# Kernel tuning notes

Hardware: AMD Instinct MI355X
Metric: run time of the kernel (lower is better)

Reference implementation:

```python
import jax, jax.numpy as jnp
import numpy as np

EPS = 1e-4

def mp_normalize(x, axis):
    # normalize() from the source: divisor = eps + ||x|| * sqrt(n_norm_elems / n_elems)
    # alpha = sqrt(norm.numel()/x.numel()) = 1/sqrt(prod of reduced dims)
    red = int(np.prod([x.shape[a] for a in axis])) if isinstance(axis, (list, tuple)) else x.shape[axis]
    w = jnp.sqrt(jnp.sum(jnp.square(x.astype(jnp.float32)), axis=axis, keepdims=True))
    w = EPS + w / np.sqrt(red)
    return x / w.astype(x.dtype)

def mp_linear(x, w, gain):
    # MP_Conv with (1,1) kernel == per-token linear; w: [out, in]
    fan_in = w.shape[1]
    wn = mp_normalize(w.astype(jnp.float32), axis=(1,)) * (gain / np.sqrt(fan_in))
    return jnp.einsum('bse,oe->bso', x, wn.astype(x.dtype))

def attention(query, gain, w_q, w_k, w_v, w_o, num_heads=16, attn_balance=0.5):
    B, S, E = query.shape
    hd = E // num_heads
    res = query
    q = mp_linear(query, w_q, gain).reshape(B, S, num_heads, hd).transpose(0, 2, 1, 3)  # bnsh
    k = mp_linear(query, w_k, gain).reshape(B, S, num_heads, hd).transpose(0, 2, 1, 3)
    v = mp_linear(query, w_v, gain).reshape(B, S, num_heads, hd).transpose(0, 2, 1, 3)
    q = mp_normalize(q, axis=(3,))
    k = mp_normalize(k, axis=(3,))
    # NOTE: contracts over sequence axis -> [B, H, hd, hd] (faithful to source einsum)
    scores = jnp.einsum('bnsh,bnsk->bnhk', q, k / np.sqrt(S))
    attn = jax.nn.softmax(scores, axis=3)
    o = jnp.einsum('bnhk,bnsk->bnsh', attn, v)  # [B, H, S, hd]
    o = o.transpose(0, 2, 1, 3).reshape(B, S, E)
    out = mp_linear(o, w_o, gain)
    t = attn_balance
    return (res * (1.0 - t) + out * t) / np.sqrt((1 - t) ** 2 + t ** 2)

def setup_inputs() -> dict:
    key = jax.random.key(0)
    ks = jax.random.split(key, 5)
    B, S, E = 4, 4096, 1024
    return {
        'query': jax.random.normal(ks[0], (B, S, E), dtype=jnp.float32),
        'gain': jnp.float32(1.0),
        'w_q': jax.random.normal(ks[1], (E, E), dtype=jnp.float32),
        'w_k': jax.random.normal(ks[2], (E, E), dtype=jnp.float32),
        'w_v': jax.random.normal(ks[3], (E, E), dtype=jnp.float32),
        'w_o': jax.random.normal(ks[4], (E, E), dtype=jnp.float32),
    }

def reference(query, gain, w_q, w_k, w_v, w_o):
    return attention(query, gain, w_q, w_k, w_v, w_o)
```

## Files before the change

### kernel.cpp

```cpp
#include <hip/hip_runtime.h>
#include <math.h>


typedef __bf16 bf16;
typedef __bf16 bf16x8 __attribute__((ext_vector_type(8)));
typedef __bf16 bf16x4 __attribute__((ext_vector_type(4)));
typedef float  f32x4  __attribute__((ext_vector_type(4)));

#define DEVINL __device__ __forceinline__

DEVINL void gload_lds16(const void* g, void* l) {
  __builtin_amdgcn_global_load_lds(
      (__attribute__((address_space(1))) void*)(void*)g,
      (__attribute__((address_space(3))) void*)l, 16, 0, 0);
}

static constexpr int Sq = 4096;
static constexpr int Ek = 1024;
static constexpr int Mrows = 16384;

__global__ __launch_bounds__(256) void k_prep_w(
    const float* __restrict__ wq, const float* __restrict__ wk,
    const float* __restrict__ wv, const float* __restrict__ wo,
    const float* __restrict__ gain_p,
    bf16* __restrict__ WN, bf16* __restrict__ WNO) {
  int r = blockIdx.x;
  int mat = r >> 10, row = r & 1023;
  const float* w = (mat == 0) ? wq : (mat == 1) ? wk : (mat == 2) ? wv : wo;
  int t = threadIdx.x;
  f32x4 v = *(const f32x4*)&w[(size_t)row * 1024 + t * 4];
  float ss = v[0]*v[0] + v[1]*v[1] + v[2]*v[2] + v[3]*v[3];
#pragma unroll
  for (int m2 = 1; m2 < 64; m2 <<= 1) ss += __shfl_xor(ss, m2);
  __shared__ float red[4];
  if ((t & 63) == 0) red[t >> 6] = ss;
  __syncthreads();
  float tot = red[0] + red[1] + red[2] + red[3];
  float g = gain_p[0];
  float scale = (g * 0.03125f) / (1e-4f + sqrtf(tot) * 0.03125f);
  bf16x4 ov;
  ov[0] = (bf16)(v[0]*scale); ov[1] = (bf16)(v[1]*scale);
  ov[2] = (bf16)(v[2]*scale); ov[3] = (bf16)(v[3]*scale);
  if (mat < 3) *(bf16x4*)&WN [(size_t)r   * 1024 + t * 4] = ov;
  else         *(bf16x4*)&WNO[(size_t)row * 1024 + t * 4] = ov;
}

__global__ __launch_bounds__(256) void k_cvt_x(const float* __restrict__ x,
                                               bf16* __restrict__ xb) {
  size_t idx = (size_t)blockIdx.x * 256 + threadIdx.x;
  const size_t n8 = (size_t)Mrows * Ek / 8;
  for (size_t i = idx; i < n8; i += (size_t)2048 * 256) {
    f32x4 a = *(const f32x4*)&x[i * 8];
    f32x4 b = *(const f32x4*)&x[i * 8 + 4];
    bf16x8 ov;
    ov[0]=(bf16)a[0]; ov[1]=(bf16)a[1]; ov[2]=(bf16)a[2]; ov[3]=(bf16)a[3];
    ov[4]=(bf16)b[0]; ov[5]=(bf16)b[1]; ov[6]=(bf16)b[2]; ov[7]=(bf16)b[3];
    *(bf16x8*)&xb[i * 8] = ov;
  }
}

template <int EPI>
__global__ __launch_bounds__(256) void k_gemm(const bf16* __restrict__ A,
                                              const bf16* __restrict__ Bw,
                                              void* __restrict__ Cout,
                                              const float* __restrict__ resid,
                                              int N) {
  constexpr int K = 1024;
  __shared__ bf16 As[128 * 32];
  __shared__ bf16 Bs[128 * 32];
  int m0 = blockIdx.y * 128, n0 = blockIdx.x * 128;
  int t = threadIdx.x, lane = t & 63, w = t >> 6;
  int wr = w >> 1, wc = w & 1;
  f32x4 acc[4][4] = {};

  const bf16* aptr0 = A  + (size_t)(m0 + (t >> 2)) * K + (t & 3) * 8;
  const bf16* bptr0 = Bw + (size_t)(n0 + (t >> 2)) * K + (t & 3) * 8;

  for (int kt = 0; kt < K / 32; ++kt) {
    __syncthreads();
    const bf16* ag = aptr0 + kt * 32;
    const bf16* bg = bptr0 + kt * 32;
    gload_lds16(ag,            &As[t * 8]);
    gload_lds16(ag + 64 * K,   &As[2048 + t * 8]);
    gload_lds16(bg,            &Bs[t * 8]);
    gload_lds16(bg + 64 * K,   &Bs[2048 + t * 8]);
    __syncthreads();

    bf16x8 af[4], bfr[4];
    int kof = (lane >> 4) * 8;
    int arow = wr * 64 + (lane & 15);
    int brow = wc * 64 + (lane & 15);
#pragma unroll
    for (int mi = 0; mi < 4; ++mi) af[mi]  = *(const bf16x8*)&As[(arow + mi * 16) * 32 + kof];
#pragma unroll
    for (int ni = 0; ni < 4; ++ni) bfr[ni] = *(const bf16x8*)&Bs[(brow + ni * 16) * 32 + kof];
#pragma unroll
    for (int mi = 0; mi < 4; ++mi)
#pragma unroll
      for (int ni = 0; ni < 4; ++ni)
        acc[mi][ni] = __builtin_amdgcn_mfma_f32_16x16x32_bf16(af[mi], bfr[ni], acc[mi][ni], 0, 0, 0);
  }

  int colbase = n0 + wc * 64 + (lane & 15);
  if constexpr (EPI == 0) {
    bf16* C = (bf16*)Cout;
    bool dn = (n0 + wc * 64) < 2048;
#pragma unroll
    for (int mi = 0; mi < 4; ++mi) {
#pragma unroll
      for (int r = 0; r < 4; ++r) {
        float scale = 1.f;
        if (dn) {
          float ss = 0.f;
#pragma unroll
          for (int ni = 0; ni < 4; ++ni) { float v = acc[mi][ni][r]; ss += v * v; }
          ss += __shfl_xor(ss, 1); ss += __shfl_xor(ss, 2);
          ss += __shfl_xor(ss, 4); ss += __shfl_xor(ss, 8);
          scale = 1.f / (1e-4f + sqrtf(ss) * 0.125f);
        }
        int row = m0 + wr * 64 + mi * 16 + ((lane >> 4) << 2) + r;
        size_t base = (size_t)row * N + colbase;
#pragma unroll
        for (int ni = 0; ni < 4; ++ni)
          C[base + ni * 16] = (bf16)(acc[mi][ni][r] * scale);
      }
    }
  } else {
    float* C = (float*)Cout;
#pragma unroll
    for (int mi = 0; mi < 4; ++mi) {
#pragma unroll
      for (int r = 0; r < 4; ++r) {
        int row = m0 + wr * 64 + mi * 16 + ((lane >> 4) << 2) + r;
        size_t base = (size_t)row * N + colbase;
#pragma unroll
        for (int ni = 0; ni < 4; ++ni) {
          size_t idx = base + ni * 16;
          C[idx] = (resid[idx] + acc[mi][ni][r]) * 0.70710678118654752f;
        }
      }
    }
  }
}

__global__ __launch_bounds__(256) void k_scores(const bf16* __restrict__ qkv,
                                                float* __restrict__ part) {
  __shared__ float Qs[64][64];
  __shared__ float Ks[64][64];
  int blk = blockIdx.x;
  int p = blk >> 6, c = blk & 63;
  int b = p >> 4, n = p & 15;
  int t = threadIdx.x;
  int j = t & 7;
  size_t rowbase = ((size_t)(b * 4096 + c * 64)) * 3072 + n * 64 + j * 8;
#pragma unroll
  for (int i = 0; i < 2; ++i) {
    int sl = i * 32 + (t >> 3);
    bf16x8 qv = *(const bf16x8*)&qkv[rowbase + (size_t)sl * 3072];
    bf16x8 kv = *(const bf16x8*)&qkv[rowbase + (size_t)sl * 3072 + 1024];
    f32x4 q0, q1, k0v, k1v;
    q0[0]=(float)qv[0]; q0[1]=(float)qv[1]; q0[2]=(float)qv[2]; q0[3]=(float)qv[3];
    q1[0]=(float)qv[4]; q1[1]=(float)qv[5]; q1[2]=(float)qv[6]; q1[3]=(float)qv[7];
    k0v[0]=(float)kv[0]; k0v[1]=(float)kv[1]; k0v[2]=(float)kv[2]; k0v[3]=(float)kv[3];
    k1v[0]=(float)kv[4]; k1v[1]=(float)kv[5]; k1v[2]=(float)kv[6]; k1v[3]=(float)kv[7];
    *(f32x4*)&Qs[sl][j * 8]     = q0;
    *(f32x4*)&Qs[sl][j * 8 + 4] = q1;
    *(f32x4*)&Ks[sl][j * 8]     = k0v;
    *(f32x4*)&Ks[sl][j * 8 + 4] = k1v;
  }
  __syncthreads();
  int h0 = (t >> 4) << 2, k0 = (t & 15) << 2;
  float acc[4][4] = {};
  for (int s = 0; s < 64; ++s) {
    f32x4 q  = *(const f32x4*)&Qs[s][h0];
    f32x4 kk = *(const f32x4*)&Ks[s][k0];
#pragma unroll
    for (int a = 0; a < 4; ++a) {
      acc[a][0] += q[a] * kk[0]; acc[a][1] += q[a] * kk[1];
      acc[a][2] += q[a] * kk[2]; acc[a][3] += q[a] * kk[3];
    }
  }
  size_t base = (size_t)blk * 4096;
#pragma unroll
  for (int a = 0; a < 4; ++a) {
    f32x4 st; st[0]=acc[a][0]; st[1]=acc[a][1]; st[2]=acc[a][2]; st[3]=acc[a][3];
    *(f32x4*)&part[base + (size_t)(h0 + a) * 64 + k0] = st;
  }
}

__global__ __launch_bounds__(256) void k_softmax(const float* __restrict__ part,
                                                 bf16* __restrict__ attn) {
  int blk = blockIdx.x;
  int p = blk >> 2, q = blk & 3;
  int t = threadIdx.x;
  int e0 = q * 1024 + t * 4;
  const float* pp = part + (size_t)p * 64 * 4096 + e0;
  f32x4 s = {};
#pragma unroll 4
  for (int c = 0; c < 64; ++c) {
    f32x4 v = *(const f32x4*)&pp[(size_t)c * 4096];
    s[0] += v[0]; s[1] += v[1]; s[2] += v[2]; s[3] += v[3];
  }
  const float sc = 1.0f / 64.0f;
  s[0] *= sc; s[1] *= sc; s[2] *= sc; s[3] *= sc;
  float mx = fmaxf(fmaxf(s[0], s[1]), fmaxf(s[2], s[3]));
  mx = fmaxf(mx, __shfl_xor(mx, 1));
  mx = fmaxf(mx, __shfl_xor(mx, 2));
  mx = fmaxf(mx, __shfl_xor(mx, 4));
  mx = fmaxf(mx, __shfl_xor(mx, 8));
  f32x4 e;
  e[0] = __expf(s[0] - mx); e[1] = __expf(s[1] - mx);
  e[2] = __expf(s[2] - mx); e[3] = __expf(s[3] - mx);
  float sum = e[0] + e[1] + e[2] + e[3];
  sum += __shfl_xor(sum, 1);
  sum += __shfl_xor(sum, 2);
  sum += __shfl_xor(sum, 4);
  sum += __shfl_xor(sum, 8);
  float inv = 1.0f / sum;
  bf16x4 ov;
  ov[0] = (bf16)(e[0] * inv); ov[1] = (bf16)(e[1] * inv);
  ov[2] = (bf16)(e[2] * inv); ov[3] = (bf16)(e[3] * inv);
  *(bf16x4*)&attn[(size_t)p * 4096 + e0] = ov;
}

__global__ __launch_bounds__(256) void k_pv(const bf16* __restrict__ qkv,
                                            const bf16* __restrict__ attn,
                                            bf16* __restrict__ o) {
  int blk = blockIdx.x;
  int p = blk >> 4, ch = blk & 15;
  int b = p >> 4, n = p & 15;
  int t = threadIdx.x, lane = t & 63, w = t >> 6;
  int s0 = ch * 256 + w * 64;
  size_t vrow0 = (size_t)(b * 4096 + s0);
  const bf16* At = attn + (size_t)p * 4096;
  f32x4 acc[4][4] = {};
#pragma unroll
  for (int ks = 0; ks < 2; ++ks) {
    int kof = ks * 32 + ((lane >> 4) << 3);
    bf16x8 vf[4], af[4];
#pragma unroll
    for (int mi = 0; mi < 4; ++mi)
      vf[mi] = *(const bf16x8*)&qkv[(vrow0 + mi * 16 + (lane & 15)) * 3072 + 2048 + n * 64 + kof];
#pragma unroll
    for (int ni = 0; ni < 4; ++ni)
      af[ni] = *(const bf16x8*)&At[(size_t)(ni * 16 + (lane & 15)) * 64 + kof];
#pragma unroll
    for (int mi = 0; mi < 4; ++mi)
#pragma unroll
      for (int ni = 0; ni < 4; ++ni)
        acc[mi][ni] = __builtin_amdgcn_mfma_f32_16x16x32_bf16(vf[mi], af[ni], acc[mi][ni], 0, 0, 0);
  }
#pragma unroll
  for (int mi = 0; mi < 4; ++mi)
#pragma unroll
    for (int r = 0; r < 4; ++r) {
      int srow = s0 + mi * 16 + ((lane >> 4) << 2) + r;
      size_t base = ((size_t)(b * 4096 + srow)) * 1024 + n * 64 + (lane & 15);
#pragma unroll
      for (int ni = 0; ni < 4; ++ni)
        o[base + ni * 16] = (bf16)acc[mi][ni][r];
    }
}

extern "C" void kernel_launch(void* const* d_in, const int* in_sizes, int n_in,
                              void* d_out, int out_size, void* d_ws, size_t ws_size,
                              hipStream_t stream) {
  const float* x    = (const float*)d_in[0];
  const float* gain = (const float*)d_in[1];
  const float* wq   = (const float*)d_in[2];
  const float* wk   = (const float*)d_in[3];
  const float* wv   = (const float*)d_in[4];
  const float* wo   = (const float*)d_in[5];

  char* ws = (char*)d_ws;
  bf16*  WN   = (bf16*)(ws + 0);
  bf16*  WNO  = (bf16*)(ws + 6291456);
  bf16*  xb   = (bf16*)(ws + 8388608);
  bf16*  qkv  = (bf16*)(ws + 41943040);
  float* part = (float*)(ws + 142606336);
  bf16*  attn = (bf16*)(ws + 209715200);
  bf16*  o    = xb;

  k_prep_w<<<4096, 256, 0, stream>>>(wq, wk, wv, wo, gain, WN, WNO);
  k_cvt_x<<<2048, 256, 0, stream>>>(x, xb);
  k_gemm<0><<<dim3(24, 128), 256, 0, stream>>>(xb, WN, (void*)qkv, nullptr, 3072);
  k_scores<<<4096, 256, 0, stream>>>(qkv, part);
  k_softmax<<<256, 256, 0, stream>>>(part, attn);
  k_pv<<<1024, 256, 0, stream>>>(qkv, attn, o);
  k_gemm<1><<<dim3(8, 128), 256, 0, stream>>>(o, WNO, d_out, x, 1024);
}
```

Measured before the change: 419.5 us.

## Replace GEMM with 256x256-tile double-buffered kernel using swizzled LDS and XCD remap

Both projection GEMMs now use a new kernel with 256x256 output tiles, 512 threads and a 64-wide K step. The K loop is double-buffered in LDS: the next tile is loaded with direct-to-LDS global loads while MFMAs run on the current one. LDS rows are XOR-swizzled to avoid bank conflicts, each iteration is split into barrier-separated phases with raised wave priority, and block IDs are remapped across the 8 XCDs for cache locality. The aim is more operand reuse and load/compute overlap than the single-buffered 128x128 kernel. The cost is about 128KB of LDS per block, which limits occupancy to one block per CU, and the out-projection launches only 256 blocks.

```diff
diff --git a/kernel.cpp b/kernel.cpp
--- a/kernel.cpp
+++ b/kernel.cpp
@@ -59,54 +59,137 @@
   }
 }
 
+
+DEVINL bf16x8 lds_frag(const bf16* base, int row, int kelem) {
+  int byte = row * 128 + kelem * 2;
+  byte ^= (row & 7) << 4;
+  return *(const bf16x8*)((const char*)base + byte);
+}
+
+#define PH_BAR() do { __builtin_amdgcn_s_barrier();                    \
+    asm volatile("s_waitcnt lgkmcnt(0)" ::: "memory");                 \
+    __builtin_amdgcn_sched_barrier(0);                                 \
+    __builtin_amdgcn_s_setprio(1); } while (0)
+#define PH_END() do { __builtin_amdgcn_s_setprio(0);                   \
+    __builtin_amdgcn_s_barrier(); } while (0)
+
 template <int EPI>
-__global__ __launch_bounds__(256) void k_gemm(const bf16* __restrict__ A,
-                                              const bf16* __restrict__ Bw,
-                                              void* __restrict__ Cout,
-                                              const float* __restrict__ resid,
-                                              int N) {
+__global__ __launch_bounds__(512, 2) void k_gemm256(
+    const bf16* __restrict__ A, const bf16* __restrict__ Bw,
+    void* __restrict__ Cout, const float* __restrict__ resid,
+    int N, int NXB) {
   constexpr int K = 1024;
-  __shared__ bf16 As[128 * 32];
-  __shared__ bf16 Bs[128 * 32];
-  int m0 = blockIdx.y * 128, n0 = blockIdx.x * 128;
-  int t = threadIdx.x, lane = t & 63, w = t >> 6;
-  int wr = w >> 1, wc = w & 1;
-  f32x4 acc[4][4] = {};
-
-  const bf16* aptr0 = A  + (size_t)(m0 + (t >> 2)) * K + (t & 3) * 8;
-  const bf16* bptr0 = Bw + (size_t)(n0 + (t >> 2)) * K + (t & 3) * 8;
-
-  for (int kt = 0; kt < K / 32; ++kt) {
-    __syncthreads();
-    const bf16* ag = aptr0 + kt * 32;
-    const bf16* bg = bptr0 + kt * 32;
-    gload_lds16(ag,            &As[t * 8]);
-    gload_lds16(ag + 64 * K,   &As[2048 + t * 8]);
-    gload_lds16(bg,            &Bs[t * 8]);
-    gload_lds16(bg + 64 * K,   &Bs[2048 + t * 8]);
-    __syncthreads();
-
-    bf16x8 af[4], bfr[4];
-    int kof = (lane >> 4) * 8;
-    int arow = wr * 64 + (lane & 15);
-    int brow = wc * 64 + (lane & 15);
-#pragma unroll
-    for (int mi = 0; mi < 4; ++mi) af[mi]  = *(const bf16x8*)&As[(arow + mi * 16) * 32 + kof];
-#pragma unroll
-    for (int ni = 0; ni < 4; ++ni) bfr[ni] = *(const bf16x8*)&Bs[(brow + ni * 16) * 32 + kof];
-#pragma unroll
-    for (int mi = 0; mi < 4; ++mi)
-#pragma unroll
-      for (int ni = 0; ni < 4; ++ni)
-        acc[mi][ni] = __builtin_amdgcn_mfma_f32_16x16x32_bf16(af[mi], bfr[ni], acc[mi][ni], 0, 0, 0);
-  }
-
-  int colbase = n0 + wc * 64 + (lane & 15);
+  constexpr int NT = K / 64;
+  __shared__ bf16 lds[2][2][256 * 64];
+
+  int nwg = gridDim.x;
+  int bid = blockIdx.x;
+  int cpx = nwg >> 3;
+  int swz = (bid & 7) * cpx + (bid >> 3);
+  int by = swz / NXB, bx = swz % NXB;
+  int m0 = by * 256, n0 = bx * 256;
+
+  int t = threadIdx.x;
+  int lane = t & 63, w = t >> 6;
+  int wr = w >> 2, wc = w & 3;
+  int fr = lane & 15;
+  int kof = (lane >> 4) * 8;
+
+  int srow = t >> 3;
+  int sslot = (t & 7) ^ (srow & 7);
+  const bf16* ag = A  + (size_t)(m0 + srow) * K + sslot * 8;
+  const bf16* bg = Bw + (size_t)(n0 + srow) * K + sslot * 8;
+
+  f32x4 acc[8][4] = {};
+
+  int cur = 0;
+  {
+    bf16* An = &lds[0][0][0];
+    bf16* Bn = &lds[0][1][0];
+#pragma unroll
+    for (int q = 0; q < 4; ++q)
+      gload_lds16(ag + (size_t)q * 64 * K, &An[q * 4096 + t * 8]);
+#pragma unroll
+    for (int q = 0; q < 4; ++q)
+      gload_lds16(bg + (size_t)q * 64 * K, &Bn[q * 4096 + t * 8]);
+    asm volatile("s_waitcnt vmcnt(0)" ::: "memory");
+    __builtin_amdgcn_s_barrier();
+  }
+
+  for (int kt = 0; kt < NT; ++kt) {
+    const bf16* Ac = &lds[cur][0][0];
+    const bf16* Bc = &lds[cur][1][0];
+    bf16* An = &lds[cur ^ 1][0][0];
+    bf16* Bn = &lds[cur ^ 1][1][0];
+    bool pf = (kt + 1 < NT);
+    int knext = (kt + 1) * 64;
+
+    bf16x8 afr[4], bfr[4];
+
+#pragma unroll
+    for (int i = 0; i < 4; ++i) bfr[i] = lds_frag(Bc, wc * 64 + i * 16 + fr, kof);
+#pragma unroll
+    for (int i = 0; i < 4; ++i) afr[i] = lds_frag(Ac, wr * 128 + i * 16 + fr, kof);
+    if (pf) {
+#pragma unroll
+      for (int q = 0; q < 4; ++q)
+        gload_lds16(ag + (size_t)q * 64 * K + knext, &An[q * 4096 + t * 8]);
+    }
+    PH_BAR();
+#pragma unroll
+    for (int mi = 0; mi < 4; ++mi)
+#pragma unroll
+      for (int ni = 0; ni < 4; ++ni)
+        acc[mi][ni] = __builtin_amdgcn_mfma_f32_16x16x32_bf16(afr[mi], bfr[ni], acc[mi][ni], 0, 0, 0);
+    PH_END();
+
+#pragma unroll
+    for (int i = 0; i < 4; ++i) afr[i] = lds_frag(Ac, wr * 128 + (4 + i) * 16 + fr, kof);
+    if (pf) {
+#pragma unroll
+      for (int q = 0; q < 4; ++q)
+        gload_lds16(bg + (size_t)q * 64 * K + knext, &Bn[q * 4096 + t * 8]);
+    }
+    PH_BAR();
+#pragma unroll
+    for (int mi = 0; mi < 4; ++mi)
+#pragma unroll
+      for (int ni = 0; ni < 4; ++ni)
+        acc[4 + mi][ni] = __builtin_amdgcn_mfma_f32_16x16x32_bf16(afr[mi], bfr[ni], acc[4 + mi][ni], 0, 0, 0);
+    PH_END();
+
+#pragma unroll
+    for (int i = 0; i < 4; ++i) bfr[i] = lds_frag(Bc, wc * 64 + i * 16 + fr, 32 + kof);
+#pragma unroll
+    for (int i = 0; i < 4; ++i) afr[i] = lds_frag(Ac, wr * 128 + i * 16 + fr, 32 + kof);
+    PH_BAR();
+#pragma unroll
+    for (int mi = 0; mi < 4; ++mi)
+#pragma unroll
+      for (int ni = 0; ni < 4; ++ni)
+        acc[mi][ni] = __builtin_amdgcn_mfma_f32_16x16x32_bf16(afr[mi], bfr[ni], acc[mi][ni], 0, 0, 0);
+    PH_END();
+
+#pragma unroll
+    for (int i = 0; i < 4; ++i) afr[i] = lds_frag(Ac, wr * 128 + (4 + i) * 16 + fr, 32 + kof);
+    PH_BAR();
+#pragma unroll
+    for (int mi = 0; mi < 4; ++mi)
+#pragma unroll
+      for (int ni = 0; ni < 4; ++ni)
+        acc[4 + mi][ni] = __builtin_amdgcn_mfma_f32_16x16x32_bf16(afr[mi], bfr[ni], acc[4 + mi][ni], 0, 0, 0);
+    __builtin_amdgcn_s_setprio(0);
+    asm volatile("s_waitcnt vmcnt(0)" ::: "memory");
+    __builtin_amdgcn_s_barrier();
+    cur ^= 1;
+  }
+
+  int colbase = n0 + wc * 64 + fr;
   if constexpr (EPI == 0) {
     bf16* C = (bf16*)Cout;
     bool dn = (n0 + wc * 64) < 2048;
 #pragma unroll
-    for (int mi = 0; mi < 4; ++mi) {
+    for (int mi = 0; mi < 8; ++mi) {
 #pragma unroll
       for (int r = 0; r < 4; ++r) {
         float scale = 1.f;
@@ -118,7 +201,7 @@
           ss += __shfl_xor(ss, 4); ss += __shfl_xor(ss, 8);
           scale = 1.f / (1e-4f + sqrtf(ss) * 0.125f);
         }
-        int row = m0 + wr * 64 + mi * 16 + ((lane >> 4) << 2) + r;
+        int row = m0 + wr * 128 + mi * 16 + ((lane >> 4) << 2) + r;
         size_t base = (size_t)row * N + colbase;
 #pragma unroll
         for (int ni = 0; ni < 4; ++ni)
@@ -128,10 +211,10 @@
   } else {
     float* C = (float*)Cout;
 #pragma unroll
-    for (int mi = 0; mi < 4; ++mi) {
+    for (int mi = 0; mi < 8; ++mi) {
 #pragma unroll
       for (int r = 0; r < 4; ++r) {
-        int row = m0 + wr * 64 + mi * 16 + ((lane >> 4) << 2) + r;
+        int row = m0 + wr * 128 + mi * 16 + ((lane >> 4) << 2) + r;
         size_t base = (size_t)row * N + colbase;
 #pragma unroll
         for (int ni = 0; ni < 4; ++ni) {
@@ -283,9 +366,9 @@
 
   k_prep_w<<<4096, 256, 0, stream>>>(wq, wk, wv, wo, gain, WN, WNO);
   k_cvt_x<<<2048, 256, 0, stream>>>(x, xb);
-  k_gemm<0><<<dim3(24, 128), 256, 0, stream>>>(xb, WN, (void*)qkv, nullptr, 3072);
+  k_gemm256<0><<<768, 512, 0, stream>>>(xb, WN, (void*)qkv, nullptr, 3072, 12);
   k_scores<<<4096, 256, 0, stream>>>(qkv, part);
   k_softmax<<<256, 256, 0, stream>>>(part, attn);
   k_pv<<<1024, 256, 0, stream>>>(qkv, attn, o);
-  k_gemm<1><<<dim3(8, 128), 256, 0, stream>>>(o, WNO, d_out, x, 1024);
-}
+  k_gemm256<1><<<256, 512, 0, stream>>>(o, WNO, d_out, x, 1024, 4);
+}
```

Result: faster. 357.6 us (-14.8%).
